# Performance work log

Measured on AMD Instinct MI355X. Metric: run time of the kernel, lower is better.

Reference implementation:

```python
import jax, jax.numpy as jnp
import numpy as np
from jax import lax

WAY = 5
SHOT = 5
TEMPERATURE = 12.5  # hard-coded in DeepEMD_Metric
EPS = 0.05          # entropic regularization for batched Sinkhorn OT
ITERS = 50          # Sinkhorn iterations


def setup_inputs() -> dict:
    key = jax.random.key(0)
    k1, k2 = jax.random.split(key)
    x1 = jax.random.normal(k1, (200, 640, 14, 14), dtype=jnp.float32)  # queries
    x2 = jax.random.normal(k2, (25, 640, 14, 14), dtype=jnp.float32)   # support: way*shot
    return {"x1": x1, "x2": x2}


def _sinkhorn_log(cost, loga, logb, eps, iters):
    # cost: [M, WAY, n, n]; loga/logb: [M, WAY, n]; returns transport plan P (rows sum to a, cols to b)
    f = jnp.zeros_like(loga)
    g = jnp.zeros_like(logb)

    def body(carry, _):
        f, g = carry
        f = eps * (loga - jax.scipy.special.logsumexp((g[..., None, :] - cost) / eps, axis=-1))
        g = eps * (logb - jax.scipy.special.logsumexp((f[..., :, None] - cost) / eps, axis=-2))
        return (f, g), None

    (f, g), _ = lax.scan(body, (f, g), None, length=iters)
    return jnp.exp((f[..., :, None] + g[..., None, :] - cost) / eps)


def reference(x1, x2):
    query = x1                                            # [M, C, H, W]
    proto = x2.reshape(WAY, SHOT, *x2.shape[1:]).mean(1)  # [WAY, C, H, W] (5-shot mean)
    M, C, H, W = query.shape
    n = H * W

    # --- weight vectors (computed on UN-normalized features, like the torch code) ---
    pooled_p = proto.mean((2, 3))  # [WAY, C]  (adaptive_avg_pool2d to 1x1)
    pooled_q = query.mean((2, 3))  # [M, C]
    w1 = jax.nn.relu(jnp.einsum('mchw,nc->mnhw', query, pooled_p).reshape(M, WAY, n)) + 1e-3
    w2 = jax.nn.relu(jnp.einsum('nchw,mc->nmhw', proto, pooled_q).reshape(WAY, M, n)) + 1e-3

    # --- center over channel dim (norm == 'center') ---
    qc = query - query.mean(1, keepdims=True)
    pc = proto - proto.mean(1, keepdims=True)

    # --- cosine similarity map [M, WAY, n_query, n_proto] without MxWAYxnxnxC repeat ---
    q = qc.reshape(M, C, n)
    p = pc.reshape(WAY, C, n)
    qn = q / jnp.maximum(jnp.linalg.norm(q, axis=1, keepdims=True), 1e-8)
    pn = p / jnp.maximum(jnp.linalg.norm(p, axis=1, keepdims=True), 1e-8)
    sim = jnp.einsum('mca,ncb->mnab', qn, pn)  # [M, WAY, n, n]

    # --- batched optimal transport (replaces per-pair OpenCV EMD loop) ---
    cost = 1.0 - sim
    a = w1 / w1.sum(-1, keepdims=True)                   # query-side marginals, sum to 1
    b = jnp.transpose(w2, (1, 0, 2))                     # [M, WAY, n]
    b = b / b.sum(-1, keepdims=True)                     # proto-side marginals, sum to 1
    P = _sinkhorn_log(cost, jnp.log(a), jnp.log(b), EPS, ITERS)

    # flow mass normalized to 1 (vs num_node in torch), so temperature/num_node * num_node = temperature
    logits = (sim * P).sum((-2, -1)) * TEMPERATURE       # [M, WAY]
    return logits
```

## Files before the change

kernel.cpp:

```cpp
#include <hip/hip_runtime.h>


#define MQ 200
#define WAYS 5
#define SHOTS 5
#define CDIM 640
#define NSP 196
#define SPAD 208
#define ITERS 50

#define RCP_EPS_LOG2E 28.853900817779268f
#define EPS_LN2 0.034657359027997264f
#define TEMP 12.5f

#define B_PF32 0u
#define B_PP   2508800u
#define B_PQ   2521600u
#define B_SP   3033600u
#define B_SP2  3037520u
#define B_SQ   3041440u
#define B_SQ2  3198240u
#define B_MP   3355040u
#define B_RP   3358960u
#define B_MQ   3362880u
#define B_RQ   3519680u
#define B_A    3676480u
#define B_B    4460480u
#define B_PF16 5244480u
#define B_QF16 7906880u
#define KCB    26624u
#define ROWB   532480u
#define WS_NEED_QPRE 114402880ull

typedef _Float16 half8 __attribute__((ext_vector_type(8)));
typedef float f32x4 __attribute__((ext_vector_type(4)));

#define PAIR_LDS 156816

__global__ __launch_bounds__(256) void k_proto(const float* __restrict__ x2, char* __restrict__ wsb) {
  float* pf32 = (float*)(wsb + B_PF32);
  float* pp   = (float*)(wsb + B_PP);
  float* sp   = (float*)(wsb + B_SP);
  float* sp2  = (float*)(wsb + B_SP2);
  __shared__ float ppl[64];
  int cg = blockIdx.x, wy = blockIdx.y, t = threadIdx.x, l = t & 63;
  if (t < 64) ppl[t] = 0.f;
  __syncthreads();
  int s = t; bool act = s < NSP;
  float as_ = 0.f, as2 = 0.f;
  int cb = cg * 64;
  for (int c = 0; c < 64; c++) {
    float p = 0.f;
    if (act) {
      const float* b0 = x2 + ((size_t)(wy * SHOTS) * CDIM + (cb + c)) * NSP + s;
      #pragma unroll
      for (int sh = 0; sh < SHOTS; sh++) p += b0[(size_t)sh * CDIM * NSP];
      p *= 0.2f;
      pf32[((size_t)wy * CDIM + cb + c) * NSP + s] = p;
      as_ += p; as2 += p * p;
    }
    float ps = p;
    #pragma unroll
    for (int off = 32; off >= 1; off >>= 1) ps += __shfl_xor(ps, off);
    if (l == 0) atomicAdd(&ppl[c], ps);
  }
  __syncthreads();
  if (act) { atomicAdd(&sp[wy * NSP + s], as_); atomicAdd(&sp2[wy * NSP + s], as2); }
  if (t < 64) pp[wy * CDIM + cb + t] = ppl[t] * (1.f / 196.f);
}

__global__ __launch_bounds__(256) void k_qstats(const float* __restrict__ x1, char* __restrict__ wsb) {
  float* pq  = (float*)(wsb + B_PQ);
  float* sq  = (float*)(wsb + B_SQ);
  float* sq2 = (float*)(wsb + B_SQ2);
  __shared__ float ppl[64];
  int cg = blockIdx.x, m = blockIdx.y, t = threadIdx.x, l = t & 63;
  if (t < 64) ppl[t] = 0.f;
  __syncthreads();
  int s = t; bool act = s < NSP;
  float as_ = 0.f, as2 = 0.f;
  int cb = cg * 64;
  const float* xb = x1 + (size_t)m * CDIM * NSP;
  for (int c = 0; c < 64; c++) {
    float p = 0.f;
    if (act) { p = xb[(size_t)(cb + c) * NSP + s]; as_ += p; as2 += p * p; }
    float ps = p;
    #pragma unroll
    for (int off = 32; off >= 1; off >>= 1) ps += __shfl_xor(ps, off);
    if (l == 0) atomicAdd(&ppl[c], ps);
  }
  __syncthreads();
  if (act) { atomicAdd(&sq[(size_t)m * NSP + s], as_); atomicAdd(&sq2[(size_t)m * NSP + s], as2); }
  if (t < 64) pq[(size_t)m * CDIM + cb + t] = ppl[t] * (1.f / 196.f);
}

__global__ __launch_bounds__(256) void k_fin(char* __restrict__ wsb) {
  int i = blockIdx.x * 256 + threadIdx.x;
  if (i < WAYS * NSP) {
    float sm = ((float*)(wsb + B_SP))[i], s2 = ((float*)(wsb + B_SP2))[i];
    float mean = sm * (1.f / CDIM);
    float var = s2 - CDIM * mean * mean;
    ((float*)(wsb + B_MP))[i] = mean;
    ((float*)(wsb + B_RP))[i] = 1.f / fmaxf(sqrtf(fmaxf(var, 0.f)), 1e-8f);
  } else if (i < WAYS * NSP + MQ * NSP) {
    int j = i - WAYS * NSP;
    float sm = ((float*)(wsb + B_SQ))[j], s2 = ((float*)(wsb + B_SQ2))[j];
    float mean = sm * (1.f / CDIM);
    float var = s2 - CDIM * mean * mean;
    ((float*)(wsb + B_MQ))[j] = mean;
    ((float*)(wsb + B_RQ))[j] = 1.f / fmaxf(sqrtf(fmaxf(var, 0.f)), 1e-8f);
  }
}

__global__ __launch_bounds__(256) void k_conv(const float* __restrict__ src,
                                              const float* __restrict__ meanA,
                                              const float* __restrict__ rnA,
                                              char* __restrict__ dst) {
  int kc = blockIdx.x, rI = blockIdx.y, t = threadIdx.x;
  const float* s0 = src + (size_t)rI * CDIM * NSP;
  const float* me = meanA + (size_t)rI * NSP;
  const float* rn = rnA + (size_t)rI * NSP;
  _Float16* d = (_Float16*)(dst + (size_t)rI * ROWB + (size_t)kc * KCB);
  int s = t;
  if (s < SPAD) {
    bool ok = s < NSP;
    float mm = ok ? me[s] : 0.f, rr = ok ? rn[s] : 0.f;
    for (int kg = 0; kg < 4; kg++) {
      half8 hv{}, lv{};
      #pragma unroll
      for (int qq = 0; qq < 8; qq++) {
        float x = 0.f;
        if (ok) x = (s0[(size_t)(kc * 32 + kg * 8 + qq) * NSP + s] - mm) * rr;
        _Float16 h = (_Float16)x;
        hv[qq] = h; lv[qq] = (_Float16)(x - (float)h);
      }
      *(half8*)&d[(kg * SPAD + s) * 8] = hv;
      *(half8*)&d[6656 + (kg * SPAD + s) * 8] = lv;
    }
  }
}

__global__ __launch_bounds__(256) void k_w1(const float* __restrict__ x1, char* __restrict__ wsb) {
  const float* pp = (const float*)(wsb + B_PP);
  float* A = (float*)(wsb + B_A);
  __shared__ float ppl[WAYS * CDIM];
  __shared__ float red[256];
  int m = blockIdx.x, t = threadIdx.x;
  for (int i = t; i < WAYS * CDIM; i += 256) ppl[i] = pp[i];
  __syncthreads();
  float acc[WAYS] = {0, 0, 0, 0, 0};
  const float* q = x1 + (size_t)m * CDIM * NSP;
  if (t < NSP) {
    for (int c = 0; c < CDIM; c++) {
      float qv = q[(size_t)c * NSP + t];
      #pragma unroll
      for (int n = 0; n < WAYS; n++) acc[n] += qv * ppl[n * CDIM + c];
    }
  }
  #pragma unroll
  for (int n = 0; n < WAYS; n++) {
    float wv = (t < NSP) ? (fmaxf(acc[n], 0.f) + 1e-3f) : 0.f;
    red[t] = wv;
    __syncthreads();
    for (int st = 128; st >= 1; st >>= 1) { if (t < st) red[t] += red[t + st]; __syncthreads(); }
    float sm = red[0];
    __syncthreads();
    if (t < NSP) A[((size_t)m * WAYS + n) * NSP + t] = wv / sm;
  }
}

__global__ __launch_bounds__(256) void k_w2(char* __restrict__ wsb) {
  const float* pf32 = (const float*)(wsb + B_PF32);
  const float* pq = (const float*)(wsb + B_PQ);
  float* B = (float*)(wsb + B_B);
  __shared__ float pql[CDIM];
  __shared__ float red[256];
  int m = blockIdx.x, t = threadIdx.x;
  for (int i = t; i < CDIM; i += 256) pql[i] = pq[(size_t)m * CDIM + i];
  __syncthreads();
  float acc[WAYS] = {0, 0, 0, 0, 0};
  if (t < NSP) {
    #pragma unroll
    for (int n = 0; n < WAYS; n++) {
      float a = 0.f;
      for (int c = 0; c < CDIM; c++) a += pf32[((size_t)n * CDIM + c) * NSP + t] * pql[c];
      acc[n] = a;
    }
  }
  #pragma unroll
  for (int n = 0; n < WAYS; n++) {
    float wv = (t < NSP) ? (fmaxf(acc[n], 0.f) + 1e-3f) : 0.f;
    red[t] = wv;
    __syncthreads();
    for (int st = 128; st >= 1; st >>= 1) { if (t < st) red[t] += red[t + st]; __syncthreads(); }
    float sm = red[0];
    __syncthreads();
    if (t < NSP) B[((size_t)m * WAYS + n) * NSP + t] = wv / sm;
  }
}

#define MFMA16(a, b, c) __builtin_amdgcn_mfma_f32_16x16x32_f16(a, b, c, 0, 0, 0)

template <bool QPRE>
__global__ __launch_bounds__(1024, 4) void k_pair(const float* __restrict__ x1,
                                                  char* __restrict__ wsb,
                                                  float* __restrict__ out) {
  extern __shared__ char smem[];
  float* Km = (float*)smem;
  float* u_l = (float*)(smem + 153664);
  float* v_l = u_l + NSP;
  float* a_l = v_l + NSP;
  float* b_l = a_l + NSP;
  float* red = (float*)(smem + 156800);

  int p = blockIdx.x, m = p / WAYS, n = p % WAYS;
  int t = threadIdx.x, w = t >> 6, l = t & 63;
  int lid = l & 15, kg4 = l >> 4;
  int WR = w >> 2, WC = w & 3;

  if (t < NSP) {
    a_l[t] = ((const float*)(wsb + B_A))[((size_t)m * WAYS + n) * NSP + t];
    b_l[t] = ((const float*)(wsb + B_B))[((size_t)m * WAYS + n) * NSP + t];
    v_l[t] = 1.f;
  }
  __syncthreads();

  const char* srcQ = wsb + B_QF16 + (size_t)m * ROWB;
  const char* srcP = wsb + B_PF16 + (size_t)n * ROWB;

  f32x4 acc[4][4];
  #pragma unroll
  for (int qi = 0; qi < 4; qi++)
    #pragma unroll
    for (int r = 0; r < 4; r++)
      #pragma unroll
      for (int e = 0; e < 4; e++) acc[qi][r][e] = 0.f;

  f32x4 st0, st1, st2, st3;

  auto STAGE_LOAD = [&](int kc) {
    if constexpr (QPRE) {
      const char* q0 = srcQ + (size_t)kc * KCB;
      const char* p0 = srcP + (size_t)kc * KCB;
      st0 = *(const f32x4*)(q0 + (size_t)t * 16);
      st1 = (t < 640) ? *(const f32x4*)(q0 + (size_t)(1024 + t) * 16)
                      : *(const f32x4*)(p0 + (size_t)(t - 640) * 16);
      st2 = *(const f32x4*)(p0 + (size_t)(384 + t) * 16);
      if (t < 256) st3 = *(const f32x4*)(p0 + (size_t)(1408 + t) * 16);
    } else {
      int kg = t >> 8, s = t & 255;
      half8 hv{}, lv{};
      if (s < SPAD) {
        bool ok = s < NSP;
        float mm = ok ? ((const float*)(wsb + B_MQ))[(size_t)m * NSP + s] : 0.f;
        float rr = ok ? ((const float*)(wsb + B_RQ))[(size_t)m * NSP + s] : 0.f;
        #pragma unroll
        for (int qq = 0; qq < 8; qq++) {
          float x = 0.f;
          if (ok) x = (x1[((size_t)m * CDIM + kc * 32 + kg * 8 + qq) * NSP + s] - mm) * rr;
          _Float16 h = (_Float16)x;
          hv[qq] = h; lv[qq] = (_Float16)(x - (float)h);
        }
      }
      st0 = __builtin_bit_cast(f32x4, hv);
      st1 = __builtin_bit_cast(f32x4, lv);
      const char* p0 = srcP + (size_t)kc * KCB;
      st2 = *(const f32x4*)(p0 + (size_t)t * 16);
      if (t < 640) st3 = *(const f32x4*)(p0 + (size_t)(1024 + t) * 16);
    }
  };
  auto STAGE_WRITE = [&](char* bufc) {
    if constexpr (QPRE) {
      *(f32x4*)(bufc + (size_t)t * 16) = st0;
      *(f32x4*)(bufc + (size_t)(1024 + t) * 16) = st1;
      *(f32x4*)(bufc + (size_t)(2048 + t) * 16) = st2;
      if (t < 256) *(f32x4*)(bufc + (size_t)(3072 + t) * 16) = st3;
    } else {
      int kg = t >> 8, s = t & 255;
      if (s < SPAD) {
        *(f32x4*)(bufc + (size_t)(kg * SPAD + s) * 16) = st0;
        *(f32x4*)(bufc + 13312 + (size_t)(kg * SPAD + s) * 16) = st1;
      }
      *(f32x4*)(bufc + 26624 + (size_t)t * 16) = st2;
      if (t < 640) *(f32x4*)(bufc + 26624 + (size_t)(1024 + t) * 16) = st3;
    }
  };

  int buf = 0;
  STAGE_LOAD(0);
  STAGE_WRITE(smem);
  __syncthreads();
  for (int kc = 0; kc < 20; kc++) {
    char* cur = smem + (size_t)buf * 53248;
    char* nxt = smem + (size_t)(buf ^ 1) * 53248;
    if (kc < 19) STAGE_LOAD(kc + 1);
    const _Float16* Ah = (const _Float16*)cur;
    const _Float16* Al = (const _Float16*)(cur + 13312);
    const _Float16* Bh = (const _Float16*)(cur + 26624);
    const _Float16* Bl = (const _Float16*)(cur + 39936);
    half8 ah[4], al[4];
    #pragma unroll
    for (int qi = 0; qi < 4; qi++) {
      int tt = WR + 4 * qi;
      if (tt < 13) {
        ah[qi] = *(const half8*)&Ah[((size_t)kg4 * SPAD + tt * 16 + lid) * 8];
        al[qi] = *(const half8*)&Al[((size_t)kg4 * SPAD + tt * 16 + lid) * 8];
      }
    }
    #pragma unroll
    for (int r = 0; r < 4; r++) {
      int jt = WC + 4 * r;
      if (jt < 13) {
        half8 bh = *(const half8*)&Bh[((size_t)kg4 * SPAD + jt * 16 + lid) * 8];
        half8 bl = *(const half8*)&Bl[((size_t)kg4 * SPAD + jt * 16 + lid) * 8];
        #pragma unroll
        for (int qi = 0; qi < 4; qi++) {
          int tt = WR + 4 * qi;
          if (tt < 13) {
            acc[qi][r] = MFMA16(ah[qi], bh, acc[qi][r]);
            acc[qi][r] = MFMA16(ah[qi], bl, acc[qi][r]);
            acc[qi][r] = MFMA16(al[qi], bh, acc[qi][r]);
          }
        }
      }
    }
    if (kc < 19) STAGE_WRITE(nxt);
    __syncthreads();
    buf ^= 1;
  }

  #pragma unroll
  for (int qi = 0; qi < 4; qi++) {
    int tt = WR + 4 * qi;
    if (tt < 13) {
      #pragma unroll
      for (int r = 0; r < 4; r++) {
        int jt = WC + 4 * r;
        if (jt < 13) {
          int j = jt * 16 + lid;
          if (j < NSP) {
            #pragma unroll
            for (int e = 0; e < 4; e++) {
              int i = tt * 16 + kg4 * 4 + e;
              if (i < NSP) Km[(size_t)i * NSP + j] = exp2f((acc[qi][r][e] - 1.f) * RCP_EPS_LOG2E);
            }
          }
        }
      }
    }
  }
  __syncthreads();

  int idx = t >> 2, hh = t & 3;
  bool act = t < 784;
  const int cb48 = 48 * hh;
  for (int it = 0; it < ITERS; it++) {
    if (act) {
      const f32x4* KmR = (const f32x4*)(Km + (size_t)idx * NSP + cb48);
      const f32x4* vR  = (const f32x4*)(v_l + cb48);
      float rs = 0.f;
      #pragma unroll
      for (int kb = 0; kb < 12; kb++) {
        f32x4 k4 = KmR[kb], v4 = vR[kb];
        rs += k4[0] * v4[0] + k4[1] * v4[1] + k4[2] * v4[2] + k4[3] * v4[3];
      }
      if (hh == 3) {
        f32x4 k4 = KmR[12], v4 = vR[12];
        rs += k4[0] * v4[0] + k4[1] * v4[1] + k4[2] * v4[2] + k4[3] * v4[3];
      }
      rs += __shfl_xor(rs, 1);
      rs += __shfl_xor(rs, 2);
      if (hh == 0) u_l[idx] = a_l[idx] / fmaxf(rs, 1e-35f);
    }
    __syncthreads();
    if (act) {
      const float* KmC = Km + idx;
      const float2* u2p = (const float2*)u_l;
      float cs = 0.f;
      #pragma unroll
      for (int k = 0; k < 24; k++) {
        float2 u2 = u2p[4 * k + hh];
        cs += KmC[(size_t)(8 * k + 2 * hh) * NSP] * u2.x;
        cs += KmC[(size_t)(8 * k + 2 * hh + 1) * NSP] * u2.y;
      }
      if (hh < 2) {
        float2 u2 = u2p[96 + hh];
        cs += KmC[(size_t)(192 + 2 * hh) * NSP] * u2.x;
        cs += KmC[(size_t)(193 + 2 * hh) * NSP] * u2.y;
      }
      cs += __shfl_xor(cs, 1);
      cs += __shfl_xor(cs, 2);
      if (hh == 0) v_l[idx] = b_l[idx] / fmaxf(cs, 1e-35f);
    }
    __syncthreads();
  }

  if (act) {
    float s4 = 0.f;
    for (int jb = hh; jb < 49; jb += 4) {
      f32x4 k4 = *(const f32x4*)&Km[(size_t)idx * NSP + jb * 4];
      f32x4 v4 = *(const f32x4*)&v_l[jb * 4];
      #pragma unroll
      for (int qq = 0; qq < 4; qq++) {
        float kk = k4[qq];
        float sim = 1.f + EPS_LN2 * log2f(kk);
        s4 += sim * kk * v4[qq];
      }
    }
    s4 += __shfl_xor(s4, 1);
    s4 += __shfl_xor(s4, 2);
    if (hh == 0) a_l[idx] = u_l[idx] * s4;
  }
  __syncthreads();
  float rv = (t < NSP) ? a_l[t] : 0.f;
  if (w < 4) {
    #pragma unroll
    for (int off = 32; off >= 1; off >>= 1) rv += __shfl_down(rv, off);
    if (l == 0) red[w] = rv;
  }
  __syncthreads();
  if (t == 0) out[p] = TEMP * (red[0] + red[1] + red[2] + red[3]);
}

extern "C" void kernel_launch(void* const* d_in, const int* in_sizes, int n_in,
                              void* d_out, int out_size, void* d_ws, size_t ws_size,
                              hipStream_t stream) {
  const float* x1 = (const float*)d_in[0];
  const float* x2 = (const float*)d_in[1];
  char* wsb = (char*)d_ws;
  float* out = (float*)d_out;
  bool qpre = ws_size >= WS_NEED_QPRE;

  hipMemsetAsync(wsb + B_SP, 0, 321440, stream);
  hipLaunchKernelGGL(k_proto, dim3(10, 5), dim3(256), 0, stream, x2, wsb);
  hipLaunchKernelGGL(k_qstats, dim3(10, 200), dim3(256), 0, stream, x1, wsb);
  hipLaunchKernelGGL(k_fin, dim3(157), dim3(256), 0, stream, wsb);
  hipLaunchKernelGGL(k_conv, dim3(20, 5), dim3(256), 0, stream,
                     (const float*)(wsb + B_PF32), (const float*)(wsb + B_MP),
                     (const float*)(wsb + B_RP), wsb + B_PF16);
  if (qpre)
    hipLaunchKernelGGL(k_conv, dim3(20, 200), dim3(256), 0, stream,
                       x1, (const float*)(wsb + B_MQ), (const float*)(wsb + B_RQ), wsb + B_QF16);
  hipLaunchKernelGGL(k_w1, dim3(MQ), dim3(256), 0, stream, x1, wsb);
  hipLaunchKernelGGL(k_w2, dim3(MQ), dim3(256), 0, stream, wsb);
  if (qpre)
    hipLaunchKernelGGL(k_pair<true>, dim3(MQ * WAYS), dim3(1024), PAIR_LDS, stream, x1, wsb, out);
  else
    hipLaunchKernelGGL(k_pair<false>, dim3(MQ * WAYS), dim3(1024), PAIR_LDS, stream, x1, wsb, out);
}
```

Before: 1.159 ms.

## Fuse w1 into query stats, split w2 over channels, cache Km in registers

The query-side weight dot products (w1) now happen inside the query-stats pass, reusing the x1 loads and accumulating with atomics. The proto-side weights (w2) move to a channel-split kernel with atomics, and a separate kernel does the relu and normalisation for both. In the Sinkhorn loop, each thread keeps its row and column slices of the kernel matrix in registers (Krow/Kcol) instead of rereading LDS every iteration. The register caching raises register pressure in a 1024-thread block, and the atomics make the weight sums nondeterministic and need an extra memset.

```diff
diff --git a/kernel.cpp b/kernel.cpp
--- a/kernel.cpp
+++ b/kernel.cpp
@@ -73,25 +73,64 @@
   float* pq  = (float*)(wsb + B_PQ);
   float* sq  = (float*)(wsb + B_SQ);
   float* sq2 = (float*)(wsb + B_SQ2);
+  float* accA = (float*)(wsb + B_A);
+  const float* pp = (const float*)(wsb + B_PP);
   __shared__ float ppl[64];
+  __shared__ float ppl2[WAYS * 64];
   int cg = blockIdx.x, m = blockIdx.y, t = threadIdx.x, l = t & 63;
+  int cb = cg * 64;
   if (t < 64) ppl[t] = 0.f;
+  for (int i = t; i < WAYS * 64; i += 256) ppl2[i] = pp[(i >> 6) * CDIM + cb + (i & 63)];
   __syncthreads();
   int s = t; bool act = s < NSP;
   float as_ = 0.f, as2 = 0.f;
-  int cb = cg * 64;
+  float aacc[WAYS] = {0, 0, 0, 0, 0};
   const float* xb = x1 + (size_t)m * CDIM * NSP;
   for (int c = 0; c < 64; c++) {
     float p = 0.f;
-    if (act) { p = xb[(size_t)(cb + c) * NSP + s]; as_ += p; as2 += p * p; }
+    if (act) {
+      p = xb[(size_t)(cb + c) * NSP + s];
+      as_ += p; as2 += p * p;
+      #pragma unroll
+      for (int n = 0; n < WAYS; n++) aacc[n] += p * ppl2[n * 64 + c];
+    }
     float ps = p;
     #pragma unroll
     for (int off = 32; off >= 1; off >>= 1) ps += __shfl_xor(ps, off);
     if (l == 0) atomicAdd(&ppl[c], ps);
   }
   __syncthreads();
-  if (act) { atomicAdd(&sq[(size_t)m * NSP + s], as_); atomicAdd(&sq2[(size_t)m * NSP + s], as2); }
+  if (act) {
+    atomicAdd(&sq[(size_t)m * NSP + s], as_);
+    atomicAdd(&sq2[(size_t)m * NSP + s], as2);
+    #pragma unroll
+    for (int n = 0; n < WAYS; n++)
+      atomicAdd(&accA[((size_t)m * WAYS + n) * NSP + s], aacc[n]);
+  }
   if (t < 64) pq[(size_t)m * CDIM + cb + t] = ppl[t] * (1.f / 196.f);
+}
+
+__global__ __launch_bounds__(256) void k_w2p(char* __restrict__ wsb) {
+  const float* pf32 = (const float*)(wsb + B_PF32);
+  const float* pq = (const float*)(wsb + B_PQ);
+  float* accB = (float*)(wsb + B_B);
+  __shared__ float pql[64];
+  int cg = blockIdx.x, m = blockIdx.y, t = threadIdx.x;
+  int cb = cg * 64;
+  if (t < 64) pql[t] = pq[(size_t)m * CDIM + cb + t];
+  __syncthreads();
+  if (t < NSP) {
+    float bacc[WAYS] = {0, 0, 0, 0, 0};
+    for (int c = 0; c < 64; c++) {
+      float pv = pql[c];
+      #pragma unroll
+      for (int n = 0; n < WAYS; n++)
+        bacc[n] += pf32[((size_t)n * CDIM + cb + c) * NSP + t] * pv;
+    }
+    #pragma unroll
+    for (int n = 0; n < WAYS; n++)
+      atomicAdd(&accB[((size_t)m * WAYS + n) * NSP + t], bacc[n]);
+  }
 }
 
 __global__ __launch_bounds__(256) void k_fin(char* __restrict__ wsb) {
@@ -112,6 +151,27 @@
   }
 }
 
+__global__ __launch_bounds__(256) void k_finm(char* __restrict__ wsb) {
+  float* A = (float*)(wsb + B_A);
+  float* B = (float*)(wsb + B_B);
+  __shared__ float red[256];
+  int p = blockIdx.x, t = threadIdx.x;
+  float av = (t < NSP) ? (fmaxf(A[(size_t)p * NSP + t], 0.f) + 1e-3f) : 0.f;
+  red[t] = av;
+  __syncthreads();
+  for (int st = 128; st >= 1; st >>= 1) { if (t < st) red[t] += red[t + st]; __syncthreads(); }
+  float sa = red[0];
+  __syncthreads();
+  if (t < NSP) A[(size_t)p * NSP + t] = av / sa;
+  float bv = (t < NSP) ? (fmaxf(B[(size_t)p * NSP + t], 0.f) + 1e-3f) : 0.f;
+  red[t] = bv;
+  __syncthreads();
+  for (int st = 128; st >= 1; st >>= 1) { if (t < st) red[t] += red[t + st]; __syncthreads(); }
+  float sb = red[0];
+  __syncthreads();
+  if (t < NSP) B[(size_t)p * NSP + t] = bv / sb;
+}
+
 __global__ __launch_bounds__(256) void k_conv(const float* __restrict__ src,
                                               const float* __restrict__ meanA,
                                               const float* __restrict__ rnA,
@@ -140,65 +200,6 @@
   }
 }
 
-__global__ __launch_bounds__(256) void k_w1(const float* __restrict__ x1, char* __restrict__ wsb) {
-  const float* pp = (const float*)(wsb + B_PP);
-  float* A = (float*)(wsb + B_A);
-  __shared__ float ppl[WAYS * CDIM];
-  __shared__ float red[256];
-  int m = blockIdx.x, t = threadIdx.x;
-  for (int i = t; i < WAYS * CDIM; i += 256) ppl[i] = pp[i];
-  __syncthreads();
-  float acc[WAYS] = {0, 0, 0, 0, 0};
-  const float* q = x1 + (size_t)m * CDIM * NSP;
-  if (t < NSP) {
-    for (int c = 0; c < CDIM; c++) {
-      float qv = q[(size_t)c * NSP + t];
-      #pragma unroll
-      for (int n = 0; n < WAYS; n++) acc[n] += qv * ppl[n * CDIM + c];
-    }
-  }
-  #pragma unroll
-  for (int n = 0; n < WAYS; n++) {
-    float wv = (t < NSP) ? (fmaxf(acc[n], 0.f) + 1e-3f) : 0.f;
-    red[t] = wv;
-    __syncthreads();
-    for (int st = 128; st >= 1; st >>= 1) { if (t < st) red[t] += red[t + st]; __syncthreads(); }
-    float sm = red[0];
-    __syncthreads();
-    if (t < NSP) A[((size_t)m * WAYS + n) * NSP + t] = wv / sm;
-  }
-}
-
-__global__ __launch_bounds__(256) void k_w2(char* __restrict__ wsb) {
-  const float* pf32 = (const float*)(wsb + B_PF32);
-  const float* pq = (const float*)(wsb + B_PQ);
-  float* B = (float*)(wsb + B_B);
-  __shared__ float pql[CDIM];
-  __shared__ float red[256];
-  int m = blockIdx.x, t = threadIdx.x;
-  for (int i = t; i < CDIM; i += 256) pql[i] = pq[(size_t)m * CDIM + i];
-  __syncthreads();
-  float acc[WAYS] = {0, 0, 0, 0, 0};
-  if (t < NSP) {
-    #pragma unroll
-    for (int n = 0; n < WAYS; n++) {
-      float a = 0.f;
-      for (int c = 0; c < CDIM; c++) a += pf32[((size_t)n * CDIM + c) * NSP + t] * pql[c];
-      acc[n] = a;
-    }
-  }
-  #pragma unroll
-  for (int n = 0; n < WAYS; n++) {
-    float wv = (t < NSP) ? (fmaxf(acc[n], 0.f) + 1e-3f) : 0.f;
-    red[t] = wv;
-    __syncthreads();
-    for (int st = 128; st >= 1; st >>= 1) { if (t < st) red[t] += red[t + st]; __syncthreads(); }
-    float sm = red[0];
-    __syncthreads();
-    if (t < NSP) B[((size_t)m * WAYS + n) * NSP + t] = wv / sm;
-  }
-}
-
 #define MFMA16(a, b, c) __builtin_amdgcn_mfma_f32_16x16x32_f16(a, b, c, 0, 0, 0)
 
 template <bool QPRE>
@@ -228,121 +229,123 @@
   const char* srcQ = wsb + B_QF16 + (size_t)m * ROWB;
   const char* srcP = wsb + B_PF16 + (size_t)n * ROWB;
 
-  f32x4 acc[4][4];
-  #pragma unroll
-  for (int qi = 0; qi < 4; qi++)
-    #pragma unroll
-    for (int r = 0; r < 4; r++)
-      #pragma unroll
-      for (int e = 0; e < 4; e++) acc[qi][r][e] = 0.f;
-
-  f32x4 st0, st1, st2, st3;
-
-  auto STAGE_LOAD = [&](int kc) {
-    if constexpr (QPRE) {
-      const char* q0 = srcQ + (size_t)kc * KCB;
-      const char* p0 = srcP + (size_t)kc * KCB;
-      st0 = *(const f32x4*)(q0 + (size_t)t * 16);
-      st1 = (t < 640) ? *(const f32x4*)(q0 + (size_t)(1024 + t) * 16)
-                      : *(const f32x4*)(p0 + (size_t)(t - 640) * 16);
-      st2 = *(const f32x4*)(p0 + (size_t)(384 + t) * 16);
-      if (t < 256) st3 = *(const f32x4*)(p0 + (size_t)(1408 + t) * 16);
-    } else {
-      int kg = t >> 8, s = t & 255;
-      half8 hv{}, lv{};
-      if (s < SPAD) {
-        bool ok = s < NSP;
-        float mm = ok ? ((const float*)(wsb + B_MQ))[(size_t)m * NSP + s] : 0.f;
-        float rr = ok ? ((const float*)(wsb + B_RQ))[(size_t)m * NSP + s] : 0.f;
+  {
+    f32x4 acc[4][4];
+    #pragma unroll
+    for (int qi = 0; qi < 4; qi++)
+      #pragma unroll
+      for (int r = 0; r < 4; r++)
         #pragma unroll
-        for (int qq = 0; qq < 8; qq++) {
-          float x = 0.f;
-          if (ok) x = (x1[((size_t)m * CDIM + kc * 32 + kg * 8 + qq) * NSP + s] - mm) * rr;
-          _Float16 h = (_Float16)x;
-          hv[qq] = h; lv[qq] = (_Float16)(x - (float)h);
-        }
-      }
-      st0 = __builtin_bit_cast(f32x4, hv);
-      st1 = __builtin_bit_cast(f32x4, lv);
-      const char* p0 = srcP + (size_t)kc * KCB;
-      st2 = *(const f32x4*)(p0 + (size_t)t * 16);
-      if (t < 640) st3 = *(const f32x4*)(p0 + (size_t)(1024 + t) * 16);
-    }
-  };
-  auto STAGE_WRITE = [&](char* bufc) {
-    if constexpr (QPRE) {
-      *(f32x4*)(bufc + (size_t)t * 16) = st0;
-      *(f32x4*)(bufc + (size_t)(1024 + t) * 16) = st1;
-      *(f32x4*)(bufc + (size_t)(2048 + t) * 16) = st2;
-      if (t < 256) *(f32x4*)(bufc + (size_t)(3072 + t) * 16) = st3;
-    } else {
-      int kg = t >> 8, s = t & 255;
-      if (s < SPAD) {
-        *(f32x4*)(bufc + (size_t)(kg * SPAD + s) * 16) = st0;
-        *(f32x4*)(bufc + 13312 + (size_t)(kg * SPAD + s) * 16) = st1;
-      }
-      *(f32x4*)(bufc + 26624 + (size_t)t * 16) = st2;
-      if (t < 640) *(f32x4*)(bufc + 26624 + (size_t)(1024 + t) * 16) = st3;
-    }
-  };
-
-  int buf = 0;
-  STAGE_LOAD(0);
-  STAGE_WRITE(smem);
-  __syncthreads();
-  for (int kc = 0; kc < 20; kc++) {
-    char* cur = smem + (size_t)buf * 53248;
-    char* nxt = smem + (size_t)(buf ^ 1) * 53248;
-    if (kc < 19) STAGE_LOAD(kc + 1);
-    const _Float16* Ah = (const _Float16*)cur;
-    const _Float16* Al = (const _Float16*)(cur + 13312);
-    const _Float16* Bh = (const _Float16*)(cur + 26624);
-    const _Float16* Bl = (const _Float16*)(cur + 39936);
-    half8 ah[4], al[4];
+        for (int e = 0; e < 4; e++) acc[qi][r][e] = 0.f;
+
+    f32x4 st0, st1, st2, st3;
+
+    auto STAGE_LOAD = [&](int kc) {
+      if constexpr (QPRE) {
+        const char* q0 = srcQ + (size_t)kc * KCB;
+        const char* p0 = srcP + (size_t)kc * KCB;
+        st0 = *(const f32x4*)(q0 + (size_t)t * 16);
+        st1 = (t < 640) ? *(const f32x4*)(q0 + (size_t)(1024 + t) * 16)
+                        : *(const f32x4*)(p0 + (size_t)(t - 640) * 16);
+        st2 = *(const f32x4*)(p0 + (size_t)(384 + t) * 16);
+        if (t < 256) st3 = *(const f32x4*)(p0 + (size_t)(1408 + t) * 16);
+      } else {
+        int kg = t >> 8, s = t & 255;
+        half8 hv{}, lv{};
+        if (s < SPAD) {
+          bool ok = s < NSP;
+          float mm = ok ? ((const float*)(wsb + B_MQ))[(size_t)m * NSP + s] : 0.f;
+          float rr = ok ? ((const float*)(wsb + B_RQ))[(size_t)m * NSP + s] : 0.f;
+          #pragma unroll
+          for (int qq = 0; qq < 8; qq++) {
+            float x = 0.f;
+            if (ok) x = (x1[((size_t)m * CDIM + kc * 32 + kg * 8 + qq) * NSP + s] - mm) * rr;
+            _Float16 h = (_Float16)x;
+            hv[qq] = h; lv[qq] = (_Float16)(x - (float)h);
+          }
+        }
+        st0 = __builtin_bit_cast(f32x4, hv);
+        st1 = __builtin_bit_cast(f32x4, lv);
+        const char* p0 = srcP + (size_t)kc * KCB;
+        st2 = *(const f32x4*)(p0 + (size_t)t * 16);
+        if (t < 640) st3 = *(const f32x4*)(p0 + (size_t)(1024 + t) * 16);
+      }
+    };
+    auto STAGE_WRITE = [&](char* bufc) {
+      if constexpr (QPRE) {
+        *(f32x4*)(bufc + (size_t)t * 16) = st0;
+        *(f32x4*)(bufc + (size_t)(1024 + t) * 16) = st1;
+        *(f32x4*)(bufc + (size_t)(2048 + t) * 16) = st2;
+        if (t < 256) *(f32x4*)(bufc + (size_t)(3072 + t) * 16) = st3;
+      } else {
+        int kg = t >> 8, s = t & 255;
+        if (s < SPAD) {
+          *(f32x4*)(bufc + (size_t)(kg * SPAD + s) * 16) = st0;
+          *(f32x4*)(bufc + 13312 + (size_t)(kg * SPAD + s) * 16) = st1;
+        }
+        *(f32x4*)(bufc + 26624 + (size_t)t * 16) = st2;
+        if (t < 640) *(f32x4*)(bufc + 26624 + (size_t)(1024 + t) * 16) = st3;
+      }
+    };
+
+    int buf = 0;
+    STAGE_LOAD(0);
+    STAGE_WRITE(smem);
+    __syncthreads();
+    for (int kc = 0; kc < 20; kc++) {
+      char* cur = smem + (size_t)buf * 53248;
+      char* nxt = smem + (size_t)(buf ^ 1) * 53248;
+      if (kc < 19) STAGE_LOAD(kc + 1);
+      const _Float16* Ah = (const _Float16*)cur;
+      const _Float16* Al = (const _Float16*)(cur + 13312);
+      const _Float16* Bh = (const _Float16*)(cur + 26624);
+      const _Float16* Bl = (const _Float16*)(cur + 39936);
+      half8 ah[4], al[4];
+      #pragma unroll
+      for (int qi = 0; qi < 4; qi++) {
+        int tt = WR + 4 * qi;
+        if (tt < 13) {
+          ah[qi] = *(const half8*)&Ah[((size_t)kg4 * SPAD + tt * 16 + lid) * 8];
+          al[qi] = *(const half8*)&Al[((size_t)kg4 * SPAD + tt * 16 + lid) * 8];
+        }
+      }
+      #pragma unroll
+      for (int r = 0; r < 4; r++) {
+        int jt = WC + 4 * r;
+        if (jt < 13) {
+          half8 bh = *(const half8*)&Bh[((size_t)kg4 * SPAD + jt * 16 + lid) * 8];
+          half8 bl = *(const half8*)&Bl[((size_t)kg4 * SPAD + jt * 16 + lid) * 8];
+          #pragma unroll
+          for (int qi = 0; qi < 4; qi++) {
+            int tt = WR + 4 * qi;
+            if (tt < 13) {
+              acc[qi][r] = MFMA16(ah[qi], bh, acc[qi][r]);
+              acc[qi][r] = MFMA16(ah[qi], bl, acc[qi][r]);
+              acc[qi][r] = MFMA16(al[qi], bh, acc[qi][r]);
+            }
+          }
+        }
+      }
+      if (kc < 19) STAGE_WRITE(nxt);
+      __syncthreads();
+      buf ^= 1;
+    }
+
     #pragma unroll
     for (int qi = 0; qi < 4; qi++) {
       int tt = WR + 4 * qi;
       if (tt < 13) {
-        ah[qi] = *(const half8*)&Ah[((size_t)kg4 * SPAD + tt * 16 + lid) * 8];
-        al[qi] = *(const half8*)&Al[((size_t)kg4 * SPAD + tt * 16 + lid) * 8];
-      }
-    }
-    #pragma unroll
-    for (int r = 0; r < 4; r++) {
-      int jt = WC + 4 * r;
-      if (jt < 13) {
-        half8 bh = *(const half8*)&Bh[((size_t)kg4 * SPAD + jt * 16 + lid) * 8];
-        half8 bl = *(const half8*)&Bl[((size_t)kg4 * SPAD + jt * 16 + lid) * 8];
         #pragma unroll
-        for (int qi = 0; qi < 4; qi++) {
-          int tt = WR + 4 * qi;
-          if (tt < 13) {
-            acc[qi][r] = MFMA16(ah[qi], bh, acc[qi][r]);
-            acc[qi][r] = MFMA16(ah[qi], bl, acc[qi][r]);
-            acc[qi][r] = MFMA16(al[qi], bh, acc[qi][r]);
-          }
-        }
-      }
-    }
-    if (kc < 19) STAGE_WRITE(nxt);
-    __syncthreads();
-    buf ^= 1;
-  }
-
-  #pragma unroll
-  for (int qi = 0; qi < 4; qi++) {
-    int tt = WR + 4 * qi;
-    if (tt < 13) {
-      #pragma unroll
-      for (int r = 0; r < 4; r++) {
-        int jt = WC + 4 * r;
-        if (jt < 13) {
-          int j = jt * 16 + lid;
-          if (j < NSP) {
-            #pragma unroll
-            for (int e = 0; e < 4; e++) {
-              int i = tt * 16 + kg4 * 4 + e;
-              if (i < NSP) Km[(size_t)i * NSP + j] = exp2f((acc[qi][r][e] - 1.f) * RCP_EPS_LOG2E);
+        for (int r = 0; r < 4; r++) {
+          int jt = WC + 4 * r;
+          if (jt < 13) {
+            int j = jt * 16 + lid;
+            if (j < NSP) {
+              #pragma unroll
+              for (int e = 0; e < 4; e++) {
+                int i = tt * 16 + kg4 * 4 + e;
+                if (i < NSP) Km[(size_t)i * NSP + j] = exp2f((acc[qi][r][e] - 1.f) * RCP_EPS_LOG2E);
+              }
             }
           }
         }
@@ -353,20 +356,29 @@
 
   int idx = t >> 2, hh = t & 3;
   bool act = t < 784;
-  const int cb48 = 48 * hh;
+  const int cb = 48 * hh;
+  f32x4 Krow[13], Kcol[13];
+  if (act) {
+    #pragma unroll
+    for (int k = 0; k < 13; k++) {
+      if (k < 12 || hh == 3) {
+        Krow[k] = *(const f32x4*)&Km[(size_t)idx * NSP + cb + 4 * k];
+        #pragma unroll
+        for (int e = 0; e < 4; e++)
+          Kcol[k][e] = Km[(size_t)(cb + 4 * k + e) * NSP + idx];
+      }
+    }
+  }
+
   for (int it = 0; it < ITERS; it++) {
     if (act) {
-      const f32x4* KmR = (const f32x4*)(Km + (size_t)idx * NSP + cb48);
-      const f32x4* vR  = (const f32x4*)(v_l + cb48);
       float rs = 0.f;
       #pragma unroll
-      for (int kb = 0; kb < 12; kb++) {
-        f32x4 k4 = KmR[kb], v4 = vR[kb];
-        rs += k4[0] * v4[0] + k4[1] * v4[1] + k4[2] * v4[2] + k4[3] * v4[3];
-      }
-      if (hh == 3) {
-        f32x4 k4 = KmR[12], v4 = vR[12];
-        rs += k4[0] * v4[0] + k4[1] * v4[1] + k4[2] * v4[2] + k4[3] * v4[3];
+      for (int k = 0; k < 13; k++) {
+        if (k < 12 || hh == 3) {
+          f32x4 v4 = *(const f32x4*)&v_l[cb + 4 * k];
+          rs += Krow[k][0] * v4[0] + Krow[k][1] * v4[1] + Krow[k][2] * v4[2] + Krow[k][3] * v4[3];
+        }
       }
       rs += __shfl_xor(rs, 1);
       rs += __shfl_xor(rs, 2);
@@ -374,19 +386,13 @@
     }
     __syncthreads();
     if (act) {
-      const float* KmC = Km + idx;
-      const float2* u2p = (const float2*)u_l;
       float cs = 0.f;
       #pragma unroll
-      for (int k = 0; k < 24; k++) {
-        float2 u2 = u2p[4 * k + hh];
-        cs += KmC[(size_t)(8 * k + 2 * hh) * NSP] * u2.x;
-        cs += KmC[(size_t)(8 * k + 2 * hh + 1) * NSP] * u2.y;
-      }
-      if (hh < 2) {
-        float2 u2 = u2p[96 + hh];
-        cs += KmC[(size_t)(192 + 2 * hh) * NSP] * u2.x;
-        cs += KmC[(size_t)(193 + 2 * hh) * NSP] * u2.y;
+      for (int k = 0; k < 13; k++) {
+        if (k < 12 || hh == 3) {
+          f32x4 u4 = *(const f32x4*)&u_l[cb + 4 * k];
+          cs += Kcol[k][0] * u4[0] + Kcol[k][1] * u4[1] + Kcol[k][2] * u4[2] + Kcol[k][3] * u4[3];
+        }
       }
       cs += __shfl_xor(cs, 1);
       cs += __shfl_xor(cs, 2);
@@ -397,14 +403,16 @@
 
   if (act) {
     float s4 = 0.f;
-    for (int jb = hh; jb < 49; jb += 4) {
-      f32x4 k4 = *(const f32x4*)&Km[(size_t)idx * NSP + jb * 4];
-      f32x4 v4 = *(const f32x4*)&v_l[jb * 4];
-      #pragma unroll
-      for (int qq = 0; qq < 4; qq++) {
-        float kk = k4[qq];
-        float sim = 1.f + EPS_LN2 * log2f(kk);
-        s4 += sim * kk * v4[qq];
+    #pragma unroll
+    for (int k = 0; k < 13; k++) {
+      if (k < 12 || hh == 3) {
+        f32x4 v4 = *(const f32x4*)&v_l[cb + 4 * k];
+        #pragma unroll
+        for (int e = 0; e < 4; e++) {
+          float kk = Krow[k][e];
+          float sim = 1.f + EPS_LN2 * log2f(kk);
+          s4 += sim * kk * v4[e];
+        }
       }
     }
     s4 += __shfl_xor(s4, 1);
@@ -432,17 +440,18 @@
   bool qpre = ws_size >= WS_NEED_QPRE;
 
   hipMemsetAsync(wsb + B_SP, 0, 321440, stream);
+  hipMemsetAsync(wsb + B_A, 0, 1568000, stream);
   hipLaunchKernelGGL(k_proto, dim3(10, 5), dim3(256), 0, stream, x2, wsb);
   hipLaunchKernelGGL(k_qstats, dim3(10, 200), dim3(256), 0, stream, x1, wsb);
+  hipLaunchKernelGGL(k_w2p, dim3(10, 200), dim3(256), 0, stream, wsb);
   hipLaunchKernelGGL(k_fin, dim3(157), dim3(256), 0, stream, wsb);
+  hipLaunchKernelGGL(k_finm, dim3(MQ * WAYS), dim3(256), 0, stream, wsb);
   hipLaunchKernelGGL(k_conv, dim3(20, 5), dim3(256), 0, stream,
                      (const float*)(wsb + B_PF32), (const float*)(wsb + B_MP),
                      (const float*)(wsb + B_RP), wsb + B_PF16);
   if (qpre)
     hipLaunchKernelGGL(k_conv, dim3(20, 200), dim3(256), 0, stream,
                        x1, (const float*)(wsb + B_MQ), (const float*)(wsb + B_RQ), wsb + B_QF16);
-  hipLaunchKernelGGL(k_w1, dim3(MQ), dim3(256), 0, stream, x1, wsb);
-  hipLaunchKernelGGL(k_w2, dim3(MQ), dim3(256), 0, stream, wsb);
   if (qpre)
     hipLaunchKernelGGL(k_pair<true>, dim3(MQ * WAYS), dim3(1024), PAIR_LDS, stream, x1, wsb, out);
   else
```

Result: faster. 1.006 ms (-13.2%).
